# Performance work log

Measured on AMD Instinct MI355X. Metric: run time of the kernel, lower is better.

## Reference

```python
import jax, jax.numpy as jnp
import numpy as np

B, CH, D, H, W = 2, 1, 10, 512, 512
BONUS = 10.0
EPS = 1e-7

C_, L_, R_ = slice(1, -1), slice(0, -2), slice(2, None)


def setup_inputs() -> dict:
    key = jax.random.key(0)
    x = jax.random.normal(key, (B, CH, D, H, W), dtype=jnp.float32)
    return {"x": x}


def _pad_rep(x):
    # replicate ('edge') padding of 1 on D,H,W, as kornia spatial_gradient3d / nms3d
    return jnp.pad(x, ((0, 0), (0, 0), (1, 1), (1, 1), (1, 1)), mode='edge')


def _forward(x, bonus=BONUS, eps=EPS):
    Dd, Hh, Ww = x.shape[-3:]
    xp = _pad_rep(x)

    # --- first-order central differences (spatial_gradient3d, mode='diff', order=1) ---
    gx = 0.5 * (xp[:, :, C_, C_, R_] - xp[:, :, C_, C_, L_])
    gy = 0.5 * (xp[:, :, C_, R_, C_] - xp[:, :, C_, L_, C_])
    gs = 0.5 * (xp[:, :, R_, C_, C_] - xp[:, :, L_, C_, C_])

    # --- second-order finite differences (order=2); cross terms scaled by 0.25 (OpenCV convention) ---
    cc = xp[:, :, C_, C_, C_]
    dxx = xp[:, :, C_, C_, L_] + xp[:, :, C_, C_, R_] - 2.0 * cc
    dyy = xp[:, :, C_, L_, C_] + xp[:, :, C_, R_, C_] - 2.0 * cc
    dss = xp[:, :, L_, C_, C_] + xp[:, :, R_, C_, C_] - 2.0 * cc
    dxy = 0.25 * (xp[:, :, C_, L_, L_] + xp[:, :, C_, R_, R_] - xp[:, :, C_, R_, L_] - xp[:, :, C_, L_, R_])
    dys = 0.25 * (xp[:, :, L_, L_, C_] + xp[:, :, R_, R_, C_] - xp[:, :, R_, L_, C_] - xp[:, :, L_, R_, C_])
    dxs = 0.25 * (xp[:, :, L_, C_, L_] + xp[:, :, R_, C_, R_] - xp[:, :, R_, C_, L_] - xp[:, :, L_, C_, R_])

    # --- strict 3x3x3 NMS: x must exceed all 26 neighbors AND 0 (kornia zeroed-center kernel) ---
    nmax = None
    for dz in range(3):
        for dyo in range(3):
            for dxo in range(3):
                if dz == 1 and dyo == 1 and dxo == 1:
                    continue
                v = xp[:, :, dz:dz + Dd, dyo:dyo + Hh, dxo:dxo + Ww]
                nmax = v if nmax is None else jnp.maximum(nmax, v)
    nmax = jnp.maximum(nmax, jnp.zeros((), x.dtype))
    m = x > nmax  # strict local maxima mask (B,CH,D,H,W)

    # --- per-voxel 3x3 solve H dx = b via Cramer's rule, only at maxima ---
    # torch adds a fixed small random |U(0,1)|*eps matrix to every Hessian to avoid singularity
    Rm = jax.random.uniform(jax.random.key(42), (3, 3), dtype=x.dtype) * eps

    ident = [[1.0, 0.0, 0.0], [0.0, 1.0, 0.0], [0.0, 0.0, 1.0]]

    def sel(h, i, j):
        # masked voxels get identity Hessian -> zero solution, safe division, clean grads
        return jnp.where(m, h + Rm[i, j], jnp.asarray(ident[i][j], x.dtype))

    h00 = sel(dxx, 0, 0); h01 = sel(dxy, 0, 1); h02 = sel(dxs, 0, 2)
    h10 = sel(dxy, 1, 0); h11 = sel(dyy, 1, 1); h12 = sel(dys, 1, 2)
    h20 = sel(dxs, 2, 0); h21 = sel(dys, 2, 1); h22 = sel(dss, 2, 2)
    z = jnp.zeros((), x.dtype)
    b0 = jnp.where(m, gx, z); b1 = jnp.where(m, gy, z); b2 = jnp.where(m, gs, z)

    c00 = h11 * h22 - h12 * h21
    c01 = h10 * h22 - h12 * h20
    c02 = h10 * h21 - h11 * h20
    det = h00 * c00 - h01 * c01 + h02 * c02
    sx = (b0 * c00 - h01 * (b1 * h22 - h12 * b2) + h02 * (b1 * h21 - h11 * b2)) / det
    sy = (h00 * (b1 * h22 - h12 * b2) - b0 * c01 + h02 * (h10 * b2 - b1 * h20)) / det
    ss = (h00 * (h11 * b2 - h21 * b1) - h01 * (h10 * b2 - h20 * b1) + b0 * c02) / det

    dx0, dx1, dx2 = -sx, -sy, -ss  # subpixel offsets (x, y, scale)

    # discard offsets far from the window center (>0.7)
    far = jnp.maximum(jnp.maximum(jnp.abs(dx0), jnp.abs(dx1)), jnp.abs(dx2)) > 0.7
    dx0 = jnp.where(far, z, dx0); dx1 = jnp.where(far, z, dx1); dx2 = jnp.where(far, z, dx2)

    # refined peak value: y = x + 0.5 * b^T dx, plus strict-maxima bonus
    dy_ = 0.5 * (gx * dx0 + gy * dx1 + gs * dx2)
    y_max = x + dy_ + bonus * m.astype(x.dtype)

    # global coordinates + subpixel offsets, channel order (scale/d, y, x)
    gd = jnp.arange(Dd, dtype=x.dtype)[:, None, None]
    gh = jnp.arange(Hh, dtype=x.dtype)[None, :, None]
    gw = jnp.arange(Ww, dtype=x.dtype)[None, None, :]
    coords_max = jnp.stack([gd + dx2, gh + dx1, gw + dx0], axis=2)  # (B,CH,3,D,H,W)
    return coords_max, y_max


def reference(x):
    return _forward(x, BONUS, EPS)
```

## Files before the change

kernel.cpp:

```cpp
#include <hip/hip_runtime.h>


constexpr int Dd = 10, Hh = 512, Ww = 512;
constexpr int HW  = Hh * Ww;
constexpr int DHW = Dd * HW;
constexpr float BONUS_F = 10.0f;

__global__ __launch_bounds__(256) void quad_kernel(
        const float* __restrict__ x, float* __restrict__ out) {
    const int tx = threadIdx.x;
    const int w0 = tx << 2;
    const int h  = (blockIdx.y << 1) + threadIdx.y;
    const int bd = blockIdx.z;
    const int d  = bd % Dd;
    const int b  = bd / Dd;

    const int pz[3] = { (d == 0) ? bd : bd - 1, bd, (d == Dd - 1) ? bd : bd + 1 };
    const int py[3] = { (h == 0) ? h : h - 1, h, (h == Hh - 1) ? h : h + 1 };
    const int wl = (w0 == 0) ? 0 : w0 - 1;
    const int wr = (w0 + 4 >= Ww) ? (Ww - 1) : (w0 + 4);

    float v[3][3][6];
#pragma unroll
    for (int zz = 0; zz < 3; ++zz) {
#pragma unroll
        for (int yy = 0; yy < 3; ++yy) {
            const float* rp = x + (size_t)pz[zz] * HW + (size_t)py[yy] * Ww;
            const float4 c = *reinterpret_cast<const float4*>(rp + w0);
            v[zz][yy][0] = rp[wl];
            v[zz][yy][1] = c.x;
            v[zz][yy][2] = c.y;
            v[zz][yy][3] = c.z;
            v[zz][yy][4] = c.w;
            v[zz][yy][5] = rp[wr];
        }
    }

    float o_d[4], o_h[4], o_w[4], o_y[4];
#pragma unroll
    for (int j = 0; j < 4; ++j) {
        const int k = j + 1;
        const float xc = v[1][1][k];

        float nm = 0.0f;
#pragma unroll
        for (int zz = 0; zz < 3; ++zz)
#pragma unroll
            for (int yy = 0; yy < 3; ++yy)
#pragma unroll
                for (int dw = -1; dw <= 1; ++dw) {
                    if (zz == 1 && yy == 1 && dw == 0) continue;
                    nm = fmaxf(nm, v[zz][yy][k + dw]);
                }
        const bool m = xc > nm;

        const float gx  = 0.5f * (v[1][1][k + 1] - v[1][1][k - 1]);
        const float gy  = 0.5f * (v[1][2][k] - v[1][0][k]);
        const float gs  = 0.5f * (v[2][1][k] - v[0][1][k]);
        const float dxx = v[1][1][k - 1] + v[1][1][k + 1] - 2.0f * xc;
        const float dyy = v[1][0][k] + v[1][2][k] - 2.0f * xc;
        const float dss = v[0][1][k] + v[2][1][k] - 2.0f * xc;
        const float dxy = 0.25f * (v[1][0][k - 1] + v[1][2][k + 1] - v[1][2][k - 1] - v[1][0][k + 1]);
        const float dys = 0.25f * (v[0][0][k] + v[2][2][k] - v[2][0][k] - v[0][2][k]);
        const float dxs = 0.25f * (v[0][1][k - 1] + v[2][1][k + 1] - v[2][1][k - 1] - v[0][1][k + 1]);

        const float c00 = dyy * dss - dys * dys;
        const float c01 = dxy * dss - dys * dxs;
        const float c02 = dxy * dys - dyy * dxs;
        const float det = dxx * c00 - dxy * c01 + dxs * c02;
        const float t1  = gy * dss - dys * gs;
        const float t2  = gy * dys - dyy * gs;
        const float t3  = dxy * gs - gy * dxs;
        const float nx = gx * c00 - dxy * t1 + dxs * t2;
        const float ny = dxx * t1 - gx * c01 + dxs * t3;
        const float ns = dxx * (-t2) - dxy * t3 + gx * c02;

        const float lim = 0.7f * fabsf(det);
        const bool keep = m && (fabsf(det) > 0.0f) &&
                          (fabsf(nx) <= lim) && (fabsf(ny) <= lim) && (fabsf(ns) <= lim);
        const float rdet = keep ? (1.0f / det) : 0.0f;
        const float dx0 = -nx * rdet;
        const float dx1 = -ny * rdet;
        const float dx2 = -ns * rdet;

        const float dy_ = 0.5f * (gx * dx0 + gy * dx1 + gs * dx2);
        const float y   = xc + dy_ + (m ? BONUS_F : 0.0f);

        o_d[j] = (float)d + dx2;
        o_h[j] = (float)h + dx1;
        o_w[j] = (float)(w0 + j) + dx0;
        o_y[j] = y;
    }

    const size_t base = (size_t)d * HW + (size_t)h * Ww + w0;
    auto pack = [](const float* s) { return make_float4(s[0], s[1], s[2], s[3]); };
    *reinterpret_cast<float4*>(out + ((size_t)(b * 3 + 0)) * DHW + base) = pack(o_d);
    *reinterpret_cast<float4*>(out + ((size_t)(b * 3 + 1)) * DHW + base) = pack(o_h);
    *reinterpret_cast<float4*>(out + ((size_t)(b * 3 + 2)) * DHW + base) = pack(o_w);
    *reinterpret_cast<float4*>(out + (size_t)6 * DHW + (size_t)b * DHW + base) = pack(o_y);
}

extern "C" void kernel_launch(void* const* d_in, const int* in_sizes, int n_in,
                              void* d_out, int out_size, void* d_ws, size_t ws_size,
                              hipStream_t stream) {
    (void)in_sizes; (void)n_in; (void)out_size; (void)d_ws; (void)ws_size;
    const float* x = (const float*)d_in[0];
    float* out = (float*)d_out;
    dim3 block(128, 2, 1);
    dim3 grid(1, Hh / 2, 2 * Dd);
    quad_kernel<<<grid, block, 0, stream>>>(x, out);
}
```

Baseline: 116.0 us.

## Switch to one voxel per thread with 64x4 2D blocks

Each thread now handles a single voxel instead of four consecutive ones. It loads its 27-point neighbourhood with scalar loads, ordered so the NMS max folds in as values arrive. The block shape becomes 64x4 over a 2D grid of W/64 by H/4 tiles, which raises the thread count and the register headroom per thread. The trade-off is that horizontal reuse of neighbour values across four outputs is lost, so more global or L2 load instructions are issued, and float4 stores are replaced by scalar coalesced stores.

Result: faster. 109.8 us (-5.4%).

```diff
diff --git a/kernel.cpp b/kernel.cpp
--- a/kernel.cpp
+++ b/kernel.cpp
@@ -8,96 +8,90 @@
 
 __global__ __launch_bounds__(256) void quad_kernel(
         const float* __restrict__ x, float* __restrict__ out) {
-    const int tx = threadIdx.x;
-    const int w0 = tx << 2;
-    const int h  = (blockIdx.y << 1) + threadIdx.y;
+    const int w  = (blockIdx.x << 6) + threadIdx.x;
+    const int h  = (blockIdx.y << 2) + threadIdx.y;
     const int bd = blockIdx.z;
     const int d  = bd % Dd;
     const int b  = bd / Dd;
 
-    const int pz[3] = { (d == 0) ? bd : bd - 1, bd, (d == Dd - 1) ? bd : bd + 1 };
-    const int py[3] = { (h == 0) ? h : h - 1, h, (h == Hh - 1) ? h : h + 1 };
-    const int wl = (w0 == 0) ? 0 : w0 - 1;
-    const int wr = (w0 + 4 >= Ww) ? (Ww - 1) : (w0 + 4);
+    const int wm = (w == 0) ? 0 : w - 1,      wp = (w == Ww - 1) ? w : w + 1;
+    const int hm = (h == 0) ? h : h - 1,      hp = (h == Hh - 1) ? h : h + 1;
+    const int zm = (d == 0) ? bd : bd - 1,    zp = (d == Dd - 1) ? bd : bd + 1;
 
-    float v[3][3][6];
-#pragma unroll
-    for (int zz = 0; zz < 3; ++zz) {
-#pragma unroll
-        for (int yy = 0; yy < 3; ++yy) {
-            const float* rp = x + (size_t)pz[zz] * HW + (size_t)py[yy] * Ww;
-            const float4 c = *reinterpret_cast<const float4*>(rp + w0);
-            v[zz][yy][0] = rp[wl];
-            v[zz][yy][1] = c.x;
-            v[zz][yy][2] = c.y;
-            v[zz][yy][3] = c.z;
-            v[zz][yy][4] = c.w;
-            v[zz][yy][5] = rp[wr];
-        }
-    }
+    const float* r0m = x + (size_t)zm * HW + (size_t)hm * Ww;
+    const float* r0c = x + (size_t)zm * HW + (size_t)h  * Ww;
+    const float* r0p = x + (size_t)zm * HW + (size_t)hp * Ww;
+    const float* r1m = x + (size_t)bd * HW + (size_t)hm * Ww;
+    const float* r1c = x + (size_t)bd * HW + (size_t)h  * Ww;
+    const float* r1p = x + (size_t)bd * HW + (size_t)hp * Ww;
+    const float* r2m = x + (size_t)zp * HW + (size_t)hm * Ww;
+    const float* r2c = x + (size_t)zp * HW + (size_t)h  * Ww;
+    const float* r2p = x + (size_t)zp * HW + (size_t)hp * Ww;
 
-    float o_d[4], o_h[4], o_w[4], o_y[4];
-#pragma unroll
-    for (int j = 0; j < 4; ++j) {
-        const int k = j + 1;
-        const float xc = v[1][1][k];
+    float nm = 0.0f;
 
-        float nm = 0.0f;
-#pragma unroll
-        for (int zz = 0; zz < 3; ++zz)
-#pragma unroll
-            for (int yy = 0; yy < 3; ++yy)
-#pragma unroll
-                for (int dw = -1; dw <= 1; ++dw) {
-                    if (zz == 1 && yy == 1 && dw == 0) continue;
-                    nm = fmaxf(nm, v[zz][yy][k + dw]);
-                }
-        const bool m = xc > nm;
+    nm = fmaxf(nm, r0m[wm]); nm = fmaxf(nm, r0m[wp]);
+    nm = fmaxf(nm, r0p[wm]); nm = fmaxf(nm, r0p[wp]);
+    const float p0_01 = r0m[w];
+    const float p0_10 = r0c[wm], p0_11 = r0c[w], p0_12 = r0c[wp];
+    const float p0_21 = r0p[w];
+    nm = fmaxf(nm, p0_01); nm = fmaxf(nm, p0_10); nm = fmaxf(nm, p0_11);
+    nm = fmaxf(nm, p0_12); nm = fmaxf(nm, p0_21);
 
-        const float gx  = 0.5f * (v[1][1][k + 1] - v[1][1][k - 1]);
-        const float gy  = 0.5f * (v[1][2][k] - v[1][0][k]);
-        const float gs  = 0.5f * (v[2][1][k] - v[0][1][k]);
-        const float dxx = v[1][1][k - 1] + v[1][1][k + 1] - 2.0f * xc;
-        const float dyy = v[1][0][k] + v[1][2][k] - 2.0f * xc;
-        const float dss = v[0][1][k] + v[2][1][k] - 2.0f * xc;
-        const float dxy = 0.25f * (v[1][0][k - 1] + v[1][2][k + 1] - v[1][2][k - 1] - v[1][0][k + 1]);
-        const float dys = 0.25f * (v[0][0][k] + v[2][2][k] - v[2][0][k] - v[0][2][k]);
-        const float dxs = 0.25f * (v[0][1][k - 1] + v[2][1][k + 1] - v[2][1][k - 1] - v[0][1][k + 1]);
+    nm = fmaxf(nm, r2m[wm]); nm = fmaxf(nm, r2m[wp]);
+    nm = fmaxf(nm, r2p[wm]); nm = fmaxf(nm, r2p[wp]);
+    const float p2_01 = r2m[w];
+    const float p2_10 = r2c[wm], p2_11 = r2c[w], p2_12 = r2c[wp];
+    const float p2_21 = r2p[w];
+    nm = fmaxf(nm, p2_01); nm = fmaxf(nm, p2_10); nm = fmaxf(nm, p2_11);
+    nm = fmaxf(nm, p2_12); nm = fmaxf(nm, p2_21);
 
-        const float c00 = dyy * dss - dys * dys;
-        const float c01 = dxy * dss - dys * dxs;
-        const float c02 = dxy * dys - dyy * dxs;
-        const float det = dxx * c00 - dxy * c01 + dxs * c02;
-        const float t1  = gy * dss - dys * gs;
-        const float t2  = gy * dys - dyy * gs;
-        const float t3  = dxy * gs - gy * dxs;
-        const float nx = gx * c00 - dxy * t1 + dxs * t2;
-        const float ny = dxx * t1 - gx * c01 + dxs * t3;
-        const float ns = dxx * (-t2) - dxy * t3 + gx * c02;
+    const float p1_00 = r1m[wm], p1_01 = r1m[w], p1_02 = r1m[wp];
+    const float p1_10 = r1c[wm], xc    = r1c[w], p1_12 = r1c[wp];
+    const float p1_20 = r1p[wm], p1_21 = r1p[w], p1_22 = r1p[wp];
+    nm = fmaxf(nm, p1_00); nm = fmaxf(nm, p1_01); nm = fmaxf(nm, p1_02);
+    nm = fmaxf(nm, p1_10);                        nm = fmaxf(nm, p1_12);
+    nm = fmaxf(nm, p1_20); nm = fmaxf(nm, p1_21); nm = fmaxf(nm, p1_22);
 
-        const float lim = 0.7f * fabsf(det);
-        const bool keep = m && (fabsf(det) > 0.0f) &&
-                          (fabsf(nx) <= lim) && (fabsf(ny) <= lim) && (fabsf(ns) <= lim);
-        const float rdet = keep ? (1.0f / det) : 0.0f;
-        const float dx0 = -nx * rdet;
-        const float dx1 = -ny * rdet;
-        const float dx2 = -ns * rdet;
+    const bool m = xc > nm;
 
-        const float dy_ = 0.5f * (gx * dx0 + gy * dx1 + gs * dx2);
-        const float y   = xc + dy_ + (m ? BONUS_F : 0.0f);
+    const float gx  = 0.5f * (p1_12 - p1_10);
+    const float gy  = 0.5f * (p1_21 - p1_01);
+    const float gs  = 0.5f * (p2_11 - p0_11);
+    const float dxx = p1_10 + p1_12 - 2.0f * xc;
+    const float dyy = p1_01 + p1_21 - 2.0f * xc;
+    const float dss = p0_11 + p2_11 - 2.0f * xc;
+    const float dxy = 0.25f * (p1_00 + p1_22 - p1_20 - p1_02);
+    const float dys = 0.25f * (p0_01 + p2_21 - p2_01 - p0_21);
+    const float dxs = 0.25f * (p0_10 + p2_12 - p2_10 - p0_12);
 
-        o_d[j] = (float)d + dx2;
-        o_h[j] = (float)h + dx1;
-        o_w[j] = (float)(w0 + j) + dx0;
-        o_y[j] = y;
-    }
+    const float c00 = dyy * dss - dys * dys;
+    const float c01 = dxy * dss - dys * dxs;
+    const float c02 = dxy * dys - dyy * dxs;
+    const float det = dxx * c00 - dxy * c01 + dxs * c02;
+    const float t1  = gy * dss - dys * gs;
+    const float t2  = gy * dys - dyy * gs;
+    const float t3  = dxy * gs - gy * dxs;
+    const float nx  = gx * c00 - dxy * t1 + dxs * t2;
+    const float ny  = dxx * t1 - gx * c01 + dxs * t3;
+    const float ns  = dxx * (-t2) - dxy * t3 + gx * c02;
 
-    const size_t base = (size_t)d * HW + (size_t)h * Ww + w0;
-    auto pack = [](const float* s) { return make_float4(s[0], s[1], s[2], s[3]); };
-    *reinterpret_cast<float4*>(out + ((size_t)(b * 3 + 0)) * DHW + base) = pack(o_d);
-    *reinterpret_cast<float4*>(out + ((size_t)(b * 3 + 1)) * DHW + base) = pack(o_h);
-    *reinterpret_cast<float4*>(out + ((size_t)(b * 3 + 2)) * DHW + base) = pack(o_w);
-    *reinterpret_cast<float4*>(out + (size_t)6 * DHW + (size_t)b * DHW + base) = pack(o_y);
+    const float lim = 0.7f * fabsf(det);
+    const bool keep = m && (fabsf(det) > 0.0f) &&
+                      (fabsf(nx) <= lim) && (fabsf(ny) <= lim) && (fabsf(ns) <= lim);
+    const float rdet = keep ? (1.0f / det) : 0.0f;
+    const float dx0 = -nx * rdet;
+    const float dx1 = -ny * rdet;
+    const float dx2 = -ns * rdet;
+
+    const float dy_ = 0.5f * (gx * dx0 + gy * dx1 + gs * dx2);
+    const float y   = xc + dy_ + (m ? BONUS_F : 0.0f);
+
+    const size_t idx = (size_t)d * HW + (size_t)h * Ww + w;
+    out[((size_t)(b * 3 + 0)) * DHW + idx] = (float)d + dx2;
+    out[((size_t)(b * 3 + 1)) * DHW + idx] = (float)h + dx1;
+    out[((size_t)(b * 3 + 2)) * DHW + idx] = (float)w + dx0;
+    out[(size_t)6 * DHW + (size_t)b * DHW + idx] = y;
 }
 
 extern "C" void kernel_launch(void* const* d_in, const int* in_sizes, int n_in,
@@ -106,7 +100,7 @@
     (void)in_sizes; (void)n_in; (void)out_size; (void)d_ws; (void)ws_size;
     const float* x = (const float*)d_in[0];
     float* out = (float*)d_out;
-    dim3 block(128, 2, 1);
-    dim3 grid(1, Hh / 2, 2 * Dd);
+    dim3 block(64, 4, 1);
+    dim3 grid(Ww / 64, Hh / 4, 2 * Dd);
     quad_kernel<<<grid, block, 0, stream>>>(x, out);
 }
```
